# Optimization experiments

Hardware: AMD Instinct MI355X
Metric: run time of the kernel (lower is better)

The kernel has to match this reference:

```python
import jax, jax.numpy as jnp
import numpy as np

B, S, H, L = 64, 512, 768, 3

def setup_inputs() -> dict:
    key = jax.random.key(0)
    ks = jax.random.split(key, 6)
    hidden = jax.random.normal(ks[0], (B, S, H), dtype=jnp.float32)
    attention_mask = jnp.ones((B, S), dtype=jnp.int32)
    labels = jax.random.randint(ks[1], (B, S), 0, L)
    W = jax.random.normal(ks[2], (H, L), dtype=jnp.float32) * 0.02
    b = jnp.zeros((L,), dtype=jnp.float32)
    start_transitions = jax.random.normal(ks[3], (L,), dtype=jnp.float32) * 0.1
    end_transitions = jax.random.normal(ks[4], (L,), dtype=jnp.float32) * 0.1
    transitions = jax.random.normal(ks[5], (L, L), dtype=jnp.float32) * 0.1
    return {"hidden": hidden, "W": W, "b": b,
            "start_transitions": start_transitions,
            "end_transitions": end_transitions,
            "transitions": transitions,
            "attention_mask": attention_mask, "labels": labels}

def _crf_nll(emissions, tags, mask, start_transitions, end_transitions, transitions):
    # emissions [B,S,L], tags [B,S] int, mask [B,S] float (contiguous, mask[:,0]=1)
    em_t = jnp.transpose(emissions, (1, 0, 2))   # [S,B,L]
    tags_t = tags.T                              # [S,B]
    mask_t = mask.T                              # [S,B]

    # --- gold-path score ---
    e0 = jnp.take_along_axis(em_t[0], tags_t[0][:, None], axis=1)[:, 0]
    score0 = start_transitions[tags_t[0]] + e0   # [B]

    def gold_step(carry, inp):
        score, prev_tags, last_tags = carry
        em, tg, m = inp
        e = jnp.take_along_axis(em, tg[:, None], axis=1)[:, 0]
        t = transitions[prev_tags, tg]
        score = score + (e + t) * m
        last_tags = jnp.where(m > 0, tg, last_tags)
        return (score, tg, last_tags), None

    (score, _, last_tags), _ = jax.lax.scan(
        gold_step, (score0, tags_t[0], tags_t[0]),
        (em_t[1:], tags_t[1:], mask_t[1:]))
    score = score + end_transitions[last_tags]   # [B]

    # --- log-partition via forward algorithm ---
    alpha0 = start_transitions[None, :] + em_t[0]  # [B,L]

    def fwd_step(alpha, inp):
        em, m = inp
        # [B,prev,next]: alpha + transition + next emission
        nxt = jax.nn.logsumexp(alpha[:, :, None] + transitions[None, :, :]
                               + em[:, None, :], axis=1)
        alpha = jnp.where(m[:, None] > 0, nxt, alpha)
        return alpha, None

    alpha, _ = jax.lax.scan(fwd_step, alpha0, (em_t[1:], mask_t[1:]))
    log_z = jax.nn.logsumexp(alpha + end_transitions[None, :], axis=1)  # [B]

    return -jnp.mean(score - log_z)  # reduction='mean', negated

def reference(hidden, W, b, start_transitions, end_transitions, transitions,
              attention_mask, labels):
    # classifier (dropout is identity in eval)
    emissions = hidden @ W + b                     # [B,S,L]
    crf_labels = jnp.where(labels < 0, 0, labels)  # masked_fill(labels<0, O)
    maskf = attention_mask.astype(emissions.dtype)
    loss = _crf_nll(emissions, crf_labels, maskf,
                    start_transitions, end_transitions, transitions)
    return loss
```

## Files before the change

kernel.cpp:

```cpp
#include <hip/hip_runtime.h>
#include <math.h>

#define HD 768
#define NL 3
#define BB 64
#define SS 512
#define NEG (-1e30f)

__device__ __forceinline__ float lse3(float x, float y, float z) {
    float m = fmaxf(fmaxf(x, y), z);
    return m + __logf(__expf(x - m) + __expf(y - m) + __expf(z - m));
}

__global__ __launch_bounds__(256) void emis_kernel(
    const float* __restrict__ hidden, const float* __restrict__ W,
    const float* __restrict__ bias, float* __restrict__ em,
    float* __restrict__ out) {
    if (blockIdx.x == 0 && threadIdx.x == 0) out[0] = 0.f;
    int gid  = blockIdx.x * blockDim.x + threadIdx.x;
    int wave = gid >> 6;
    int lane = threadIdx.x & 63;
    int BS = BB * SS;
    if (wave >= BS) return;
    const float4* h4 = (const float4*)(hidden + (size_t)wave * HD);
    float a0 = 0.f, a1 = 0.f, a2 = 0.f;
#pragma unroll
    for (int i = 0; i < 3; ++i) {
        int k4 = lane + 64 * i;
        float4 v = h4[k4];
        int k = k4 * 4;
        a0 = fmaf(v.x, W[(k + 0) * 3 + 0], a0);
        a1 = fmaf(v.x, W[(k + 0) * 3 + 1], a1);
        a2 = fmaf(v.x, W[(k + 0) * 3 + 2], a2);
        a0 = fmaf(v.y, W[(k + 1) * 3 + 0], a0);
        a1 = fmaf(v.y, W[(k + 1) * 3 + 1], a1);
        a2 = fmaf(v.y, W[(k + 1) * 3 + 2], a2);
        a0 = fmaf(v.z, W[(k + 2) * 3 + 0], a0);
        a1 = fmaf(v.z, W[(k + 2) * 3 + 1], a1);
        a2 = fmaf(v.z, W[(k + 2) * 3 + 2], a2);
        a0 = fmaf(v.w, W[(k + 3) * 3 + 0], a0);
        a1 = fmaf(v.w, W[(k + 3) * 3 + 1], a1);
        a2 = fmaf(v.w, W[(k + 3) * 3 + 2], a2);
    }
#pragma unroll
    for (int off = 32; off; off >>= 1) {
        a0 += __shfl_down(a0, off);
        a1 += __shfl_down(a1, off);
        a2 += __shfl_down(a2, off);
    }
    if (lane == 0) {
        int b = wave >> 9;
        int s = wave & (SS - 1);
        float* o = em + ((size_t)b * SS + s) * NL;
        o[0] = a0 + bias[0];
        o[1] = a1 + bias[1];
        o[2] = a2 + bias[2];
    }
}

__global__ __launch_bounds__(256) void crf_fused_kernel(
    const float* __restrict__ em,
    const int* __restrict__ mask,
    const int* __restrict__ labels,
    const float* __restrict__ startT, const float* __restrict__ endT,
    const float* __restrict__ trans, float* __restrict__ out) {
    int b = blockIdx.x;
    int w = threadIdx.x >> 6;
    int l = threadIdx.x & 63;
    int s0 = w * 128 + l * 2;

    float T00 = trans[0], T01 = trans[1], T02 = trans[2];
    float T10 = trans[3], T11 = trans[4], T12 = trans[5];
    float T20 = trans[6], T21 = trans[7], T22 = trans[8];

    const float* emb = em + (size_t)b * SS * NL;
    const int*   tg  = labels + b * SS;
    const int*   mk  = mask + b * SS;

    const float2* e2 = (const float2*)(emb + (size_t)s0 * NL);
    float2 v01 = e2[0], v23 = e2[1], v45 = e2[2];
    int2 tt = *(const int2*)(tg + s0);
    int2 mm = *(const int2*)(mk + s0);
    int pv = (s0 > 0) ? tg[s0 - 1] : 0;
    int prev = pv < 0 ? 0 : pv;

    float P00, P01, P02, P10, P11, P12, P20, P21, P22;
    float gold = 0.f;
    int last_s = -1, last_t = 0;

#define GOLD(kk, ee0, ee1, ee2, tv, mv, ACT)                                   \
    int t = (tv) < 0 ? 0 : (tv);                                               \
    bool act = (ACT) && ((mv) != 0);                                           \
    {                                                                          \
        float ev = (t == 0) ? (ee0) : ((t == 1) ? (ee1) : (ee2));              \
        float r0 = (t == 0) ? T00 : ((t == 1) ? T01 : T02);                    \
        float r1 = (t == 0) ? T10 : ((t == 1) ? T11 : T12);                    \
        float r2 = (t == 0) ? T20 : ((t == 1) ? T21 : T22);                    \
        float tpt = (prev == 0) ? r0 : ((prev == 1) ? r1 : r2);                \
        gold += act ? (ev + tpt) : 0.f;                                        \
        last_t = act ? t : last_t;                                             \
        last_s = act ? (s0 + (kk)) : last_s;                                   \
        prev = t;                                                              \
    }

#define STEP0(ee0, ee1, ee2, tv, mv) {                                         \
    GOLD(0, ee0, ee1, ee2, tv, mv, (s0 > 0))                                   \
    P00 = act ? (T00 + (ee0)) : 0.f;                                           \
    P01 = act ? (T01 + (ee1)) : NEG;                                           \
    P02 = act ? (T02 + (ee2)) : NEG;                                           \
    P10 = act ? (T10 + (ee0)) : NEG;                                           \
    P11 = act ? (T11 + (ee1)) : 0.f;                                           \
    P12 = act ? (T12 + (ee2)) : NEG;                                           \
    P20 = act ? (T20 + (ee0)) : NEG;                                           \
    P21 = act ? (T21 + (ee1)) : NEG;                                           \
    P22 = act ? (T22 + (ee2)) : 0.f;                                           \
}

#define STEPK(kk, ee0, ee1, ee2, tv, mv) {                                     \
    GOLD(kk, ee0, ee1, ee2, tv, mv, true)                                      \
    float n00 = lse3(P00 + T00, P01 + T10, P02 + T20) + (ee0);                 \
    float n01 = lse3(P00 + T01, P01 + T11, P02 + T21) + (ee1);                 \
    float n02 = lse3(P00 + T02, P01 + T12, P02 + T22) + (ee2);                 \
    float n10 = lse3(P10 + T00, P11 + T10, P12 + T20) + (ee0);                 \
    float n11 = lse3(P10 + T01, P11 + T11, P12 + T21) + (ee1);                 \
    float n12 = lse3(P10 + T02, P11 + T12, P12 + T22) + (ee2);                 \
    float n20 = lse3(P20 + T00, P21 + T10, P22 + T20) + (ee0);                 \
    float n21 = lse3(P20 + T01, P21 + T11, P22 + T21) + (ee1);                 \
    float n22 = lse3(P20 + T02, P21 + T12, P22 + T22) + (ee2);                 \
    P00 = act ? n00 : P00; P01 = act ? n01 : P01; P02 = act ? n02 : P02;       \
    P10 = act ? n10 : P10; P11 = act ? n11 : P11; P12 = act ? n12 : P12;       \
    P20 = act ? n20 : P20; P21 = act ? n21 : P21; P22 = act ? n22 : P22;       \
}

    STEP0(    v01.x, v01.y, v23.x, tt.x, mm.x)
    STEPK(1,  v23.y, v45.x, v45.y, tt.y, mm.y)

#pragma unroll
    for (int off = 1; off < 64; off <<= 1) {
        float B00 = __shfl_down(P00, off), B01 = __shfl_down(P01, off);
        float B02 = __shfl_down(P02, off), B10 = __shfl_down(P10, off);
        float B11 = __shfl_down(P11, off), B12 = __shfl_down(P12, off);
        float B20 = __shfl_down(P20, off), B21 = __shfl_down(P21, off);
        float B22 = __shfl_down(P22, off);
        float n00 = lse3(P00 + B00, P01 + B10, P02 + B20);
        float n01 = lse3(P00 + B01, P01 + B11, P02 + B21);
        float n02 = lse3(P00 + B02, P01 + B12, P02 + B22);
        float n10 = lse3(P10 + B00, P11 + B10, P12 + B20);
        float n11 = lse3(P10 + B01, P11 + B11, P12 + B21);
        float n12 = lse3(P10 + B02, P11 + B12, P12 + B22);
        float n20 = lse3(P20 + B00, P21 + B10, P22 + B20);
        float n21 = lse3(P20 + B01, P21 + B11, P22 + B21);
        float n22 = lse3(P20 + B02, P21 + B12, P22 + B22);
        P00 = n00; P01 = n01; P02 = n02;
        P10 = n10; P11 = n11; P12 = n12;
        P20 = n20; P21 = n21; P22 = n22;

        gold += __shfl_down(gold, off);
        int os = __shfl_down(last_s, off);
        int ot = __shfl_down(last_t, off);
        if (os > last_s) { last_s = os; last_t = ot; }
    }

    __shared__ float lds[4][12];
    if (l == 0) {
        lds[w][0] = P00; lds[w][1] = P01; lds[w][2] = P02;
        lds[w][3] = P10; lds[w][4] = P11; lds[w][5] = P12;
        lds[w][6] = P20; lds[w][7] = P21; lds[w][8] = P22;
        lds[w][9] = gold;
        lds[w][10] = __int_as_float(last_s);
        lds[w][11] = __int_as_float(last_t);
    }
    __syncthreads();

    if (threadIdx.x == 0) {
        float R00 = lds[0][0], R01 = lds[0][1], R02 = lds[0][2];
        float R10 = lds[0][3], R11 = lds[0][4], R12 = lds[0][5];
        float R20 = lds[0][6], R21 = lds[0][7], R22 = lds[0][8];
        float g  = lds[0][9];
        int ls = __float_as_int(lds[0][10]), lt = __float_as_int(lds[0][11]);
#pragma unroll
        for (int c = 1; c < 4; ++c) {
            float B00 = lds[c][0], B01 = lds[c][1], B02 = lds[c][2];
            float B10 = lds[c][3], B11 = lds[c][4], B12 = lds[c][5];
            float B20 = lds[c][6], B21 = lds[c][7], B22 = lds[c][8];
            float n00 = lse3(R00 + B00, R01 + B10, R02 + B20);
            float n01 = lse3(R00 + B01, R01 + B11, R02 + B21);
            float n02 = lse3(R00 + B02, R01 + B12, R02 + B22);
            float n10 = lse3(R10 + B00, R11 + B10, R12 + B20);
            float n11 = lse3(R10 + B01, R11 + B11, R12 + B21);
            float n12 = lse3(R10 + B02, R11 + B12, R12 + B22);
            float n20 = lse3(R20 + B00, R21 + B10, R22 + B20);
            float n21 = lse3(R20 + B01, R21 + B11, R22 + B21);
            float n22 = lse3(R20 + B02, R21 + B12, R22 + B22);
            R00 = n00; R01 = n01; R02 = n02;
            R10 = n10; R11 = n11; R12 = n12;
            R20 = n20; R21 = n21; R22 = n22;
            g += lds[c][9];
            int os = __float_as_int(lds[c][10]);
            int ot = __float_as_int(lds[c][11]);
            if (os > ls) { ls = os; lt = ot; }
        }

        float e00 = emb[0], e01 = emb[1], e02 = emb[2];
        int t0 = tg[0]; t0 = t0 < 0 ? 0 : t0;
        float st0 = startT[0], st1 = startT[1], st2 = startT[2];
        float en0 = endT[0],   en1 = endT[1],   en2 = endT[2];

        float al0 = st0 + e00, al1 = st1 + e01, al2 = st2 + e02;
        float f0 = lse3(al0 + R00, al1 + R10, al2 + R20);
        float f1 = lse3(al0 + R01, al1 + R11, al2 + R21);
        float f2 = lse3(al0 + R02, al1 + R12, al2 + R22);
        float logZ = lse3(f0 + en0, f1 + en1, f2 + en2);
        float sc0 = ((t0 == 0) ? st0 : ((t0 == 1) ? st1 : st2)) +
                    ((t0 == 0) ? e00 : ((t0 == 1) ? e01 : e02));
        if (ls < 0) lt = t0;
        float endv = (lt == 0) ? en0 : ((lt == 1) ? en1 : en2);
        float contrib = logZ - (sc0 + g + endv);
        atomicAdd(out, contrib * (1.0f / BB));
    }
}

extern "C" void kernel_launch(void* const* d_in, const int* in_sizes, int n_in,
                              void* d_out, int out_size, void* d_ws, size_t ws_size,
                              hipStream_t stream) {
    const float* hidden = (const float*)d_in[0];
    const float* W      = (const float*)d_in[1];
    const float* bias   = (const float*)d_in[2];
    const float* startT = (const float*)d_in[3];
    const float* endT   = (const float*)d_in[4];
    const float* trans  = (const float*)d_in[5];
    const int*   mask   = (const int*)d_in[6];
    const int*   labels = (const int*)d_in[7];
    float* out = (float*)d_out;

    float* em = (float*)d_ws;

    int BS = BB * SS;
    int blocks = BS / 4;
    emis_kernel<<<blocks, 256, 0, stream>>>(hidden, W, bias, em, out);
    crf_fused_kernel<<<BB, 256, 0, stream>>>(em, mask, labels, startT, endT,
                                             trans, out);
}
```

Baseline: 30.46 us.

## Process four tokens per wave in emission GEMV and pad emissions to float4

```diff
diff --git a/kernel.cpp b/kernel.cpp
--- a/kernel.cpp
+++ b/kernel.cpp
@@ -19,14 +19,16 @@
     if (blockIdx.x == 0 && threadIdx.x == 0) out[0] = 0.f;
     int gid  = blockIdx.x * blockDim.x + threadIdx.x;
     int wave = gid >> 6;
-    int lane = threadIdx.x & 63;
-    int BS = BB * SS;
-    if (wave >= BS) return;
-    const float4* h4 = (const float4*)(hidden + (size_t)wave * HD);
+    int l    = threadIdx.x & 63;
+    int q    = l & 15;
+    int sub  = l >> 4;
+    int tok  = wave * 4 + sub;
+
+    const float4* h4 = (const float4*)(hidden + (size_t)tok * HD);
     float a0 = 0.f, a1 = 0.f, a2 = 0.f;
 #pragma unroll
-    for (int i = 0; i < 3; ++i) {
-        int k4 = lane + 64 * i;
+    for (int i = 0; i < 12; ++i) {
+        int k4 = q + 16 * i;
         float4 v = h4[k4];
         int k = k4 * 4;
         a0 = fmaf(v.x, W[(k + 0) * 3 + 0], a0);
@@ -43,18 +45,16 @@
         a2 = fmaf(v.w, W[(k + 3) * 3 + 2], a2);
     }
 #pragma unroll
-    for (int off = 32; off; off >>= 1) {
+    for (int off = 8; off; off >>= 1) {
         a0 += __shfl_down(a0, off);
         a1 += __shfl_down(a1, off);
         a2 += __shfl_down(a2, off);
     }
-    if (lane == 0) {
-        int b = wave >> 9;
-        int s = wave & (SS - 1);
-        float* o = em + ((size_t)b * SS + s) * NL;
-        o[0] = a0 + bias[0];
-        o[1] = a1 + bias[1];
-        o[2] = a2 + bias[2];
+    if (q == 0) {
+        int b = tok >> 9;
+        int s = tok & (SS - 1);
+        float4 o = {a0 + bias[0], a1 + bias[1], a2 + bias[2], 0.f};
+        ((float4*)em)[(size_t)b * SS + s] = o;
     }
 }
 
@@ -73,12 +73,12 @@
     float T10 = trans[3], T11 = trans[4], T12 = trans[5];
     float T20 = trans[6], T21 = trans[7], T22 = trans[8];
 
-    const float* emb = em + (size_t)b * SS * NL;
+    const float* emb = em + (size_t)b * SS * 4;
     const int*   tg  = labels + b * SS;
     const int*   mk  = mask + b * SS;
 
-    const float2* e2 = (const float2*)(emb + (size_t)s0 * NL);
-    float2 v01 = e2[0], v23 = e2[1], v45 = e2[2];
+    const float4* ep4 = (const float4*)emb;
+    float4 Ea = ep4[s0], Eb = ep4[s0 + 1];
     int2 tt = *(const int2*)(tg + s0);
     int2 mm = *(const int2*)(mk + s0);
     int pv = (s0 > 0) ? tg[s0 - 1] : 0;
@@ -132,8 +132,8 @@
     P20 = act ? n20 : P20; P21 = act ? n21 : P21; P22 = act ? n22 : P22;       \
 }
 
-    STEP0(    v01.x, v01.y, v23.x, tt.x, mm.x)
-    STEPK(1,  v23.y, v45.x, v45.y, tt.y, mm.y)
+    STEP0(    Ea.x, Ea.y, Ea.z, tt.x, mm.x)
+    STEPK(1,  Eb.x, Eb.y, Eb.z, tt.y, mm.y)
 
 #pragma unroll
     for (int off = 1; off < 64; off <<= 1) {
@@ -235,9 +235,7 @@
 
     float* em = (float*)d_ws;
 
-    int BS = BB * SS;
-    int blocks = BS / 4;
-    emis_kernel<<<blocks, 256, 0, stream>>>(hidden, W, bias, em, out);
+    emis_kernel<<<2048, 256, 0, stream>>>(hidden, W, bias, em, out);
     crf_fused_kernel<<<BB, 256, 0, stream>>>(em, mask, labels, startT, endT,
                                              trans, out);
 }
```

Result: slower. 31.27 us (+2.7%).
